# Kernel optimization log

Measured on AMD Instinct MI355X. Metric: run time of the kernel, lower is better.

The kernel has to match this reference:

```python
import jax, jax.numpy as jnp
import numpy as np

B, S, D, H, NUM_LABELS = 16, 1024, 1024, 16, 3
LN_EPS = 1e-5


def setup_inputs() -> dict:
    key = jax.random.key(0)
    ks = iter(jax.random.split(key, 16))

    def w(shape, k):
        return jax.random.normal(k, shape, jnp.float32) * 0.02

    inp = {}
    inp["embedded"] = jax.random.normal(next(ks), (B, S, D), jnp.float32)
    inp["attention_mask"] = jnp.ones((B, S), jnp.float32)
    for pfx in ("p2h", "h2p"):
        for name in ("q", "k", "v", "o"):
            inp[f"{pfx}_W{name}"] = w((D, D), next(ks))
            inp[f"{pfx}_b{name}"] = jnp.zeros((D,), jnp.float32)
        inp[f"{pfx}_ln_g"] = jnp.ones((D,), jnp.float32)
        inp[f"{pfx}_ln_b"] = jnp.zeros((D,), jnp.float32)
    inp["W1"] = w((4 * D, D), next(ks)); inp["b1"] = jnp.zeros((D,), jnp.float32)
    inp["W2"] = w((D, D // 2), next(ks)); inp["b2"] = jnp.zeros((D // 2,), jnp.float32)
    inp["W3"] = w((D // 2, NUM_LABELS), next(ks)); inp["b3"] = jnp.zeros((NUM_LABELS,), jnp.float32)
    return inp


def _layernorm(x, g, b):
    mu = jnp.mean(x, axis=-1, keepdims=True)
    var = jnp.mean(jnp.square(x - mu), axis=-1, keepdims=True)
    return (x - mu) / jnp.sqrt(var + LN_EPS) * g + b


def _cross_attn(q_in, kv_in, kv_mask, Wq, bq, Wk, bk, Wv, bv, Wo, bo, g, bln):
    Bs, Sq, Dm = q_in.shape
    Sk = kv_in.shape[1]
    hd = Dm // H
    Q = (q_in @ Wq + bq).reshape(Bs, Sq, H, hd)
    K = (kv_in @ Wk + bk).reshape(Bs, Sk, H, hd)
    V = (kv_in @ Wv + bv).reshape(Bs, Sk, H, hd)
    scores = jnp.einsum("bqhd,bkhd->bhqk", Q, K) / jnp.sqrt(jnp.float32(hd))
    scores = jnp.where(kv_mask[:, None, None, :] == 0, jnp.float32(-1e9), scores)
    wts = jax.nn.softmax(scores, axis=-1)  # dropout is identity in eval
    att = jnp.einsum("bhqk,bkhd->bqhd", wts, V).reshape(Bs, Sq, Dm)
    return _layernorm(att @ Wo + bo + q_in, g, bln)


def _pool(x, m):
    s = jnp.sum(x * m[:, :, None], axis=1)
    d = jnp.clip(jnp.sum(m, axis=1, keepdims=True), 1e-9, None)
    return s / d


def reference(embedded, attention_mask,
              p2h_Wq, p2h_bq, p2h_Wk, p2h_bk, p2h_Wv, p2h_bv, p2h_Wo, p2h_bo, p2h_ln_g, p2h_ln_b,
              h2p_Wq, h2p_bq, h2p_Wk, h2p_bk, h2p_Wv, h2p_bv, h2p_Wo, h2p_bo, h2p_ln_g, h2p_ln_b,
              W1, b1, W2, b2, W3, b3):
    half = embedded.shape[1] // 2
    premise, hypothesis = embedded[:, :half], embedded[:, half:]
    pm, hm = attention_mask[:, :half], attention_mask[:, half:]
    p2h = _cross_attn(premise, hypothesis, hm,
                      p2h_Wq, p2h_bq, p2h_Wk, p2h_bk, p2h_Wv, p2h_bv, p2h_Wo, p2h_bo, p2h_ln_g, p2h_ln_b)
    h2p = _cross_attn(hypothesis, premise, pm,
                      h2p_Wq, h2p_bq, h2p_Wk, h2p_bk, h2p_Wv, h2p_bv, h2p_Wo, h2p_bo, h2p_ln_g, h2p_ln_b)
    feats = jnp.concatenate([_pool(premise, pm), _pool(hypothesis, hm),
                             _pool(p2h, pm), _pool(h2p, hm)], axis=-1)
    h1 = jax.nn.relu(feats @ W1 + b1)
    h2 = jax.nn.relu(h1 @ W2 + b2)
    return h2 @ W3 + b3
```

## Files before the change

### kernel.cpp

```cpp
#include <hip/hip_runtime.h>
#include <hip/hip_bf16.h>

typedef __attribute__((ext_vector_type(8))) __bf16 bf16x8;
typedef __attribute__((ext_vector_type(4))) float f32x4;
typedef __attribute__((ext_vector_type(4))) int i32x4;
typedef __attribute__((ext_vector_type(4))) unsigned short u16x4;

#define MFMA16(a, b, c) __builtin_amdgcn_mfma_f32_16x16x32_bf16((a), (b), (c), 0, 0, 0)

__device__ __forceinline__ void gload_lds16(const void* g, void* l)
{
    __builtin_amdgcn_global_load_lds(
        (const __attribute__((address_space(1))) unsigned int*)g,
        (__attribute__((address_space(3))) unsigned int*)l, 16, 0, 0);
}

struct LnW { const float* g[2]; const float* b[2]; };

__global__ __launch_bounds__(256) void cast_emb_kernel(const float* __restrict__ emb,
                                                       __bf16* __restrict__ A)
{
    int i = (blockIdx.x * 256 + threadIdx.x) * 4;
    int r = i >> 10, d = i & 1023;
    size_t src = ((size_t)(r >> 9) * 1024 + (r & 511)) * 1024 + d;
    f32x4 p = *(const f32x4*)(emb + src);
    f32x4 h = *(const f32x4*)(emb + src + 512 * 1024);
    union { __bf16 b[4]; u16x4 u; } cp, ch;
#pragma unroll
    for (int j = 0; j < 4; ++j) { cp.b[j] = (__bf16)p[j]; ch.b[j] = (__bf16)h[j]; }
    *(u16x4*)(A + i) = cp.u;
    *(u16x4*)(A + 8388608 + i) = ch.u;
}

struct WPtrs { const float* p[8]; };
__global__ __launch_bounds__(256) void cast_wt_kernel(WPtrs wp, __bf16* __restrict__ Wt0)
{
    const float* W = wp.p[blockIdx.z];
    __bf16* Wt = Wt0 + (size_t)blockIdx.z * 1048576;
    __shared__ float tile[32][33];
    int n0 = blockIdx.x * 32, k0 = blockIdx.y * 32;
    int tx = threadIdx.x, ty = threadIdx.y;
#pragma unroll
    for (int i = ty; i < 32; i += 8)
        tile[i][tx] = W[(size_t)(k0 + i) * 1024 + n0 + tx];
    __syncthreads();
#pragma unroll
    for (int i = ty; i < 32; i += 8)
        Wt[(size_t)(n0 + i) * 1024 + k0 + tx] = (__bf16)tile[tx][i];
}

struct GArgs {
    const __bf16* w[2];
    const float* bias[6];
    __bf16* Qb; __bf16* Kb; __bf16* Vt;
    float* Cf; const float* resid;
};
template <int EPI>
__global__ __launch_bounds__(256, 3) void gemm_bt(const __bf16* __restrict__ A, GArgs a,
                                                  int NN)
{
    __shared__ __align__(16) __bf16 As[128 * 32];
    __shared__ __align__(16) __bf16 Bs[128 * 32];
    const int t = threadIdx.x;
    const int l = t & 63, w = t >> 6;
    const int wr = w >> 1, wc = w & 1;
    const int lrow = l & 15, lk = l >> 4;

    const int id = blockIdx.x;
    const int x = id & 7, rr = id >> 3;
    const int mblk = x * 16 + (rr & 15);
    const int nblk = rr >> 4;
    const int m0 = mblk * 128, n0 = nblk * 128;
    const int dir = mblk >> 6;
    const int seg = (EPI == 5) ? (n0 >> 10) : 0;
    const int r0 = t >> 2, kc0 = (t & 3) * 8;
    const int K = 1024;

    const int am0 = (EPI == 5 && seg != 0) ? (m0 ^ 8192) : m0;
    const __bf16* Bt = a.w[dir];
    const __bf16* gA0 = A + (size_t)(am0 + r0) * K + kc0;
    const __bf16* gA1 = gA0 + (size_t)64 * K;
    const __bf16* gB0 = Bt + (size_t)(n0 + r0) * K + kc0;
    const __bf16* gB1 = gB0 + (size_t)64 * K;
    __bf16* dA0 = &As[r0 * 32 + kc0];
    __bf16* dA1 = &As[(r0 + 64) * 32 + kc0];
    __bf16* dB0 = &Bs[r0 * 32 + kc0];
    __bf16* dB1 = &Bs[(r0 + 64) * 32 + kc0];

    const f32x4 zero = {0.f, 0.f, 0.f, 0.f};
    f32x4 acc[4][4];
#pragma unroll
    for (int mi = 0; mi < 4; ++mi)
#pragma unroll
        for (int ni = 0; ni < 4; ++ni) acc[mi][ni] = zero;

    for (int kt = 0; kt < 32; ++kt) {
        const int ko = kt * 32;
        gload_lds16(gA0 + ko, dA0);
        gload_lds16(gA1 + ko, dA1);
        gload_lds16(gB0 + ko, dB0);
        gload_lds16(gB1 + ko, dB1);
        __syncthreads();
        bf16x8 af[4], bfv[4];
#pragma unroll
        for (int mi = 0; mi < 4; ++mi)
            af[mi] = *(const bf16x8*)(&As[(wr * 64 + mi * 16 + lrow) * 32 + lk * 8]);
#pragma unroll
        for (int ni = 0; ni < 4; ++ni)
            bfv[ni] = *(const bf16x8*)(&Bs[(wc * 64 + ni * 16 + lrow) * 32 + lk * 8]);
#pragma unroll
        for (int mi = 0; mi < 4; ++mi)
#pragma unroll
            for (int ni = 0; ni < 4; ++ni)
                acc[mi][ni] = MFMA16(af[mi], bfv[ni], acc[mi][ni]);
        __syncthreads();
    }

    const float* bsel = a.bias[dir * 3 + seg];
#pragma unroll
    for (int mi = 0; mi < 4; ++mi) {
#pragma unroll
        for (int ni = 0; ni < 4; ++ni) {
            int col = n0 + wc * 64 + ni * 16 + lrow;
            int c2 = col & 1023;
            float bv = bsel[c2];
#pragma unroll
            for (int r = 0; r < 4; ++r) {
                int row = m0 + wr * 64 + mi * 16 + lk * 4 + r;
                float v = acc[mi][ni][r] + bv;
                if (EPI == 5) {
                    if (seg == 0) {
                        a.Qb[(size_t)row * 1024 + c2] = (__bf16)v;
                    } else if (seg == 1) {
                        a.Kb[(size_t)row * 1024 + c2] = (__bf16)v;
                    } else {
                        int local = row & 8191;
                        int b_ = local >> 9, pos = local & 511;
                        int h_ = c2 >> 6, hd = c2 & 63;
                        a.Vt[(size_t)dir * 8388608 +
                             (((size_t)(b_ * 16 + h_) * 64 + hd) << 9) + pos] = (__bf16)v;
                    }
                } else {
                    int local = row & 8191;
                    int b_ = local >> 9, s = local & 511;
                    float rv = a.resid[((size_t)b_ * 1024 + dir * 512 + s) * 1024 + c2];
                    a.Cf[(size_t)row * 1024 + c2] = v + rv;
                }
            }
        }
    }
}

__global__ __launch_bounds__(256, 3) void attn_kernel(const __bf16* __restrict__ Q,
                                                      const __bf16* __restrict__ Kb,
                                                      const __bf16* __restrict__ Vt,
                                                      const float* __restrict__ mask,
                                                      __bf16* __restrict__ att)
{
    __shared__ __align__(16) __bf16 KB[2][128 * 64];
    __shared__ __align__(16) __bf16 Pt[64 * 128];
    __shared__ __align__(16) float msk[512];
    const int id = blockIdx.x;
    const int xcd = id & 7, slot = id >> 3;
    const int dirbh = xcd * 64 + (slot >> 3);
    const int q0 = (slot & 7) * 64;
    const int dir = dirbh >> 8, bh = dirbh & 255;
    const int b = bh >> 4, h = bh & 15;
    const int mask_half = dir ? 0 : 512;
    const int tid = threadIdx.x, l = tid & 63, w = tid >> 6;
    const int lrow = l & 15, lk = l >> 4;
    const size_t rowbase = (size_t)dir * 8192 + b * 512;

    const __bf16* kbase = Kb + rowbase * 1024 + h * 64;
    const __bf16* vsrc = Vt + (size_t)dir * 8388608 + (size_t)bh * 64 * 512;

    auto stage = [&](int t, int buf) {
        char* dst = (char*)KB[buf];
#pragma unroll
        for (int i = 0; i < 4; ++i) {
            int c = tid + i * 256;
            int pos = c >> 3, gslot = (c & 7) ^ (pos & 7);
            gload_lds16(kbase + (size_t)(t * 128 + pos) * 1024 + gslot * 8, dst + c * 16);
        }
    };

    stage(0, 0);
    for (int i = tid; i < 512; i += 256) msk[i] = mask[b * 1024 + mask_half + i];

    const __bf16* qptr = Q + (rowbase + q0 + w * 16 + lrow) * 1024 + h * 64;
    bf16x8 qf0 = *(const bf16x8*)(qptr + lk * 8);
    bf16x8 qf1 = *(const bf16x8*)(qptr + 32 + lk * 8);

    const f32x4 zero = {0.f, 0.f, 0.f, 0.f};
    f32x4 av[4];
#pragma unroll
    for (int ni = 0; ni < 4; ++ni) av[ni] = zero;
    float m_run = -3e38f, su = 0.f;
    const int psw = lrow & 7;
    char* prowp = (char*)Pt + (w * 16 + lrow) * 256;
    f32x4 sc[8];
    bf16x8 vfr[16];

#pragma unroll
    for (int t = 0; t < 4; ++t) {
        __syncthreads();
        const char* kbuf = (const char*)KB[t & 1];
#pragma unroll
        for (int jj = 0; jj < 8; ++jj) {
            const char* kb = kbuf + (jj * 16 + lrow) * 128;
            bf16x8 k0 = *(const bf16x8*)(kb + ((lk ^ psw) << 4));
            bf16x8 k1 = *(const bf16x8*)(kb + (((lk + 4) ^ psw) << 4));
            f32x4 c = zero;
            c = MFMA16(k0, qf0, c);
            c = MFMA16(k1, qf1, c);
            sc[jj] = c;
        }
        if (t < 3) stage(t + 1, (t + 1) & 1);

        const int koff = t * 128;
#pragma unroll
        for (int ks = 0; ks < 4; ++ks)
#pragma unroll
            for (int ni = 0; ni < 4; ++ni)
                vfr[ks * 4 + ni] =
                    *(const bf16x8*)(&vsrc[(ni * 16 + lrow) * 512 + koff + ks * 32 + lk * 8]);

        float mt = -3e38f;
#pragma unroll
        for (int jj = 0; jj < 8; ++jj) {
            f32x4 mv = *(const f32x4*)(&msk[koff + jj * 16 + lk * 4]);
#pragma unroll
            for (int r = 0; r < 4; ++r) {
                float s = sc[jj][r] * 0.125f;
                if (mv[r] == 0.f) s = -1e9f;
                sc[jj][r] = s;
                mt = fmaxf(mt, s);
            }
        }
        mt = fmaxf(mt, __shfl_xor(mt, 16));
        mt = fmaxf(mt, __shfl_xor(mt, 32));
        float m_new = fmaxf(m_run, mt);
        float f = __expf(m_run - m_new);
        float s0 = 0.f, s1 = 0.f;
#pragma unroll
        for (int jj = 0; jj < 8; ++jj) {
            float e0 = __expf(sc[jj][0] - m_new);
            float e1 = __expf(sc[jj][1] - m_new);
            float e2 = __expf(sc[jj][2] - m_new);
            float e3 = __expf(sc[jj][3] - m_new);
            sc[jj][0] = e0; sc[jj][1] = e1; sc[jj][2] = e2; sc[jj][3] = e3;
            s0 += e0 + e1;
            s1 += e2 + e3;
        }
        float ssum = s0 + s1;
        ssum += __shfl_xor(ssum, 16);
        ssum += __shfl_xor(ssum, 32);
        su = su * f + ssum;
        m_run = m_new;
#pragma unroll
        for (int r = 0; r < 4; ++r) {
            float fr = __shfl(f, (l & 48) | (lk * 4 + r));
#pragma unroll
            for (int ni = 0; ni < 4; ++ni) av[ni][r] *= fr;
        }

#pragma unroll
        for (int jj = 0; jj < 8; ++jj) {
            union { __bf16 b[4]; unsigned long long u; } pk;
#pragma unroll
            for (int r = 0; r < 4; ++r) pk.b[r] = (__bf16)sc[jj][r];
            int slot2 = jj * 2 + (lk >> 1);
            *(unsigned long long*)(prowp + (((slot2 ^ psw) << 4) | ((lk & 1) << 3))) = pk.u;
        }
#pragma unroll
        for (int ks = 0; ks < 4; ++ks) {
            bf16x8 pf = *(const bf16x8*)(prowp + (((ks * 4 + lk) ^ psw) << 4));
#pragma unroll
            for (int ni = 0; ni < 4; ++ni)
                av[ni] = MFMA16(pf, vfr[ks * 4 + ni], av[ni]);
        }
    }

    const float inv = 1.f / su;
#pragma unroll
    for (int r = 0; r < 4; ++r) {
        float ivr = __shfl(inv, (l & 48) | (lk * 4 + r));
        size_t orow = rowbase + q0 + w * 16 + lk * 4 + r;
#pragma unroll
        for (int ni = 0; ni < 4; ++ni)
            att[orow * 1024 + h * 64 + ni * 16 + lrow] = (__bf16)(av[ni][r] * ivr);
    }
}

__global__ __launch_bounds__(256) void ln_stats_kernel(const float* __restrict__ X,
                                                       float2* __restrict__ stats)
{
    const int r = blockIdx.x, t = threadIdx.x;
    const float* x = X + (size_t)r * 1024;
    f32x4 v = *(const f32x4*)(x + t * 4);
    float s = v[0] + v[1] + v[2] + v[3];
    float q = v[0] * v[0] + v[1] * v[1] + v[2] * v[2] + v[3] * v[3];
#pragma unroll
    for (int d = 1; d < 64; d <<= 1) { s += __shfl_xor(s, d); q += __shfl_xor(q, d); }
    __shared__ float rs[4], rq[4];
    if ((t & 63) == 0) { rs[t >> 6] = s; rq[t >> 6] = q; }
    __syncthreads();
    if (t == 0) {
        s = rs[0] + rs[1] + rs[2] + rs[3];
        q = rq[0] + rq[1] + rq[2] + rq[3];
        float mu = s * (1.f / 1024.f);
        float var = q * (1.f / 1024.f) - mu * mu;
        stats[r] = make_float2(mu, rsqrtf(var + 1e-5f));
    }
}

__global__ __launch_bounds__(256) void pool_f32_kernel(const float* __restrict__ X,
                                                       const float* __restrict__ mask,
                                                       float* __restrict__ feats)
{
    const int b = blockIdx.y, d0 = blockIdx.x * 64, half = blockIdx.z * 512;
    const int t = threadIdx.x, d = d0 + (t & 63), sl = t >> 6;
    float acc = 0.f, ms = 0.f;
#pragma unroll 4
    for (int s = sl * 128; s < sl * 128 + 128; ++s) {
        float m = mask[b * 1024 + half + s];
        acc += X[((size_t)b * 1024 + half + s) * 1024 + d] * m;
        ms += m;
    }
    __shared__ float ra[4][64];
    __shared__ float rm[4];
    ra[sl][t & 63] = acc;
    if ((t & 63) == 0) rm[sl] = ms;
    __syncthreads();
    if (t < 64) {
        float a = ra[0][t] + ra[1][t] + ra[2][t] + ra[3][t];
        float m = rm[0] + rm[1] + rm[2] + rm[3];
        feats[b * 4096 + blockIdx.z * 1024 + d0 + t] = a / fmaxf(m, 1e-9f);
    }
}

__global__ __launch_bounds__(256) void pool_ln_kernel(const float* __restrict__ Of,
                                                      const float2* __restrict__ stats,
                                                      const float* __restrict__ mask,
                                                      LnW lw,
                                                      float* __restrict__ feats)
{
    const int b = blockIdx.y, d0 = blockIdx.x * 64, dir = blockIdx.z;
    const int half = dir * 512;
    const int t = threadIdx.x, d = d0 + (t & 63), sl = t >> 6;
    float acc = 0.f, ms = 0.f;
#pragma unroll 4
    for (int s = sl * 128; s < sl * 128 + 128; ++s) {
        float m = mask[b * 1024 + half + s];
        int row = dir * 8192 + b * 512 + s;
        float2 st = stats[row];
        float x = Of[(size_t)row * 1024 + d];
        acc += m * (x - st.x) * st.y;
        ms += m;
    }
    __shared__ float ra[4][64];
    __shared__ float rm[4];
    ra[sl][t & 63] = acc;
    if ((t & 63) == 0) rm[sl] = ms;
    __syncthreads();
    if (t < 64) {
        float a = ra[0][t] + ra[1][t] + ra[2][t] + ra[3][t];
        float m = rm[0] + rm[1] + rm[2] + rm[3];
        float g = lw.g[dir][d0 + t], bb = lw.b[dir][d0 + t];
        feats[b * 4096 + 2048 + dir * 1024 + d0 + t] = (g * a + bb * m) / fmaxf(m, 1e-9f);
    }
}

__global__ __launch_bounds__(256) void fc_init_kernel(const float* __restrict__ b1,
                                                      const float* __restrict__ b2,
                                                      float* __restrict__ h1,
                                                      float* __restrict__ h2)
{
    int i = blockIdx.x * 256 + threadIdx.x;
    if (i < 16 * 1024) h1[i] = b1[i & 1023];
    else h2[i - 16 * 1024] = b2[(i - 16 * 1024) & 511];
}

template <int CH, int RELU_IN>
__global__ __launch_bounds__(256) void fc_atomic_kernel(const float* __restrict__ in,
                                                        const float* __restrict__ W,
                                                        float* __restrict__ out,
                                                        int IF, int OF)
{
    __shared__ float ins[16 * CH];
    const int t = threadIdx.x;
    const int col = blockIdx.x * 256 + t;
    const int i0 = blockIdx.y * CH;
#pragma unroll
    for (int idx = t; idx < 16 * CH; idx += 256) {
        int b = idx / CH, i = idx % CH;
        float v = in[b * IF + i0 + i];
        if (RELU_IN) v = fmaxf(v, 0.f);
        ins[idx] = v;
    }
    __syncthreads();
    float acc[16];
#pragma unroll
    for (int b = 0; b < 16; ++b) acc[b] = 0.f;
#pragma unroll 4
    for (int i = 0; i < CH; ++i) {
        float wv = W[(size_t)(i0 + i) * OF + col];
#pragma unroll
        for (int b = 0; b < 16; ++b) acc[b] += ins[b * CH + i] * wv;
    }
#pragma unroll
    for (int b = 0; b < 16; ++b) atomicAdd(out + b * OF + col, acc[b]);
}

__global__ __launch_bounds__(64) void mlp3_kernel(const float* __restrict__ h2,
                                                  const float* __restrict__ W3,
                                                  const float* __restrict__ b3,
                                                  float* __restrict__ out)
{
    int b = blockIdx.x, t = threadIdx.x;
    float a0 = 0.f, a1 = 0.f, a2 = 0.f;
    for (int i = t; i < 512; i += 64) {
        float hv = fmaxf(h2[b * 512 + i], 0.f);
        a0 += hv * W3[i * 3 + 0];
        a1 += hv * W3[i * 3 + 1];
        a2 += hv * W3[i * 3 + 2];
    }
#pragma unroll
    for (int d = 1; d < 64; d <<= 1) {
        a0 += __shfl_xor(a0, d);
        a1 += __shfl_xor(a1, d);
        a2 += __shfl_xor(a2, d);
    }
    if (t == 0) {
        out[b * 3 + 0] = a0 + b3[0];
        out[b * 3 + 1] = a1 + b3[1];
        out[b * 3 + 2] = a2 + b3[2];
    }
}

extern "C" void kernel_launch(void* const* d_in, const int* in_sizes, int n_in,
                              void* d_out, int out_size, void* d_ws, size_t ws_size,
                              hipStream_t stream)
{
    const float* emb  = (const float*)d_in[0];
    const float* mask = (const float*)d_in[1];
    const float* W1 = (const float*)d_in[22];
    const float* b1 = (const float*)d_in[23];
    const float* W2 = (const float*)d_in[24];
    const float* b2 = (const float*)d_in[25];
    const float* W3 = (const float*)d_in[26];
    const float* b3 = (const float*)d_in[27];

    char* ws = (char*)d_ws;
    constexpr size_t MB = 1ull << 20;
    __bf16* A     = (__bf16*)(ws);
    __bf16* Wt    = (__bf16*)(ws + 32 * MB);
    __bf16* Qb    = (__bf16*)(ws + 48 * MB);
    __bf16* Kb    = (__bf16*)(ws + 80 * MB);
    __bf16* Vt    = (__bf16*)(ws + 112 * MB);
    __bf16* attb  = (__bf16*)(ws);
    float*  Of    = (float*) (ws + 48 * MB);
    float*  feats = (float*) (ws + 144 * MB);
    float*  h1    = (float*) (ws + 144 * MB + 512 * 1024);
    float*  h2    = (float*) (ws + 145 * MB);
    float2* stats = (float2*)(ws + 146 * MB);

    cast_emb_kernel<<<8192, 256, 0, stream>>>(emb, A);
    WPtrs wp;
    const int widx[8] = {2, 4, 6, 8, 12, 14, 16, 18};
    for (int i = 0; i < 8; ++i) wp.p[i] = (const float*)d_in[widx[i]];
    cast_wt_kernel<<<dim3(32, 32, 8), dim3(32, 8), 0, stream>>>(wp, Wt);

    GArgs gqkv = {}, go = {};
    LnW lw;
    for (int dir = 0; dir < 2; ++dir) {
        const int base = dir ? 12 : 2;
        gqkv.w[dir] = Wt + (size_t)(dir * 4) * 1048576;
        gqkv.bias[dir * 3 + 0] = (const float*)d_in[base + 1];
        gqkv.bias[dir * 3 + 1] = (const float*)d_in[base + 3];
        gqkv.bias[dir * 3 + 2] = (const float*)d_in[base + 5];
        go.w[dir] = Wt + (size_t)(dir * 4 + 3) * 1048576;
        go.bias[dir * 3] = (const float*)d_in[base + 7];
        lw.g[dir] = (const float*)d_in[base + 8];
        lw.b[dir] = (const float*)d_in[base + 9];
    }
    gqkv.Qb = Qb; gqkv.Kb = Kb; gqkv.Vt = Vt;
    go.Cf = Of; go.resid = emb;

    gemm_bt<5><<<3072, 256, 0, stream>>>(A, gqkv, 24);
    attn_kernel<<<4096, 256, 0, stream>>>(Qb, Kb, Vt, mask, attb);
    gemm_bt<2><<<1024, 256, 0, stream>>>(attb, go, 8);
    ln_stats_kernel<<<16384, 256, 0, stream>>>(Of, stats);
    pool_ln_kernel<<<dim3(16, 16, 2), 256, 0, stream>>>(Of, stats, mask, lw, feats);
    pool_f32_kernel<<<dim3(16, 16, 2), 256, 0, stream>>>(emb, mask, feats);

    fc_init_kernel<<<96, 256, 0, stream>>>(b1, b2, h1, h2);
    fc_atomic_kernel<128, 0><<<dim3(4, 32), 256, 0, stream>>>(feats, W1, h1, 4096, 1024);
    fc_atomic_kernel<32, 1><<<dim3(2, 32), 256, 0, stream>>>(h1, W2, h2, 1024, 512);
    mlp3_kernel<<<16, 64, 0, stream>>>(h2, W3, b3, (float*)d_out);
}
```

Before: 502.5 us.

## Replace QKV GEMM with 256x256-tile double-buffered swizzled-LDS kernel

Adds a dedicated QKV projection kernel using 256x256 output tiles, 512 threads, a K-step of 64, and double-buffered LDS with XOR swizzling. Next-tile loads are staged in four quarters interleaved with MFMA phases, and s_setprio is raised around the MFMA blocks. The aim is more data reuse per tile, fewer bank conflicts and overlap of global loads with compute. The generic gemm_bt is simplified to serve only the output projection. The trade-off is 128KB of LDS per block, which lowers occupancy, and a small grid of 768 blocks.

```diff
diff --git a/kernel.cpp b/kernel.cpp
--- a/kernel.cpp
+++ b/kernel.cpp
@@ -55,6 +55,172 @@
     __bf16* Qb; __bf16* Kb; __bf16* Vt;
     float* Cf; const float* resid;
 };
+
+__global__ __launch_bounds__(512, 2) void gemm256_qkv(const __bf16* __restrict__ A, GArgs a)
+{
+    __shared__ __align__(16) __bf16 Ab[2][256 * 64];
+    __shared__ __align__(16) __bf16 Bb[2][256 * 64];
+    const int tid = threadIdx.x, l = tid & 63;
+    const int wid = tid >> 6, wm = wid >> 2, wn = wid & 3;
+    const int lrow = l & 15, lk = l >> 4;
+
+    const int id = blockIdx.x;
+    const int x = id & 7, rr = id >> 3;
+    const int mblk = x * 8 + (rr & 7);
+    const int nblk = rr >> 3;
+    const int m0 = mblk * 256, n0 = nblk * 256;
+    const int dir = mblk >> 5;
+    const int seg = n0 >> 10;
+    const int am0 = (seg != 0) ? (m0 ^ 8192) : m0;
+    const __bf16* Ap = A + (size_t)am0 * 1024;
+    const __bf16* Bp = a.w[dir] + (size_t)n0 * 1024;
+
+    auto stage = [&](int kt, int b, int hp) {
+        const __bf16* gp = (hp < 2) ? Ap : Bp;
+        __bf16* lp = ((hp < 2) ? Ab[b] : Bb[b]) + (hp & 1) * (128 * 64);
+#pragma unroll
+        for (int i = 0; i < 2; ++i) {
+            int cc = tid + i * 512;
+            int rl = cc >> 3, sl = cc & 7;
+            int gs = sl ^ (rl & 7);
+            gload_lds16(gp + (size_t)((hp & 1) * 128 + rl) * 1024 + kt * 64 + gs * 8,
+                        lp + cc * 8);
+        }
+    };
+
+    stage(0, 0, 0); stage(0, 0, 1); stage(0, 0, 2); stage(0, 0, 3);
+
+    const f32x4 zero = {0.f, 0.f, 0.f, 0.f};
+    f32x4 acc[8][4];
+#pragma unroll
+    for (int mi = 0; mi < 8; ++mi)
+#pragma unroll
+        for (int ni = 0; ni < 4; ++ni) acc[mi][ni] = zero;
+
+    bf16x8 af[4][2], bf[2][2];
+
+    for (int kt = 0; kt < 16; ++kt) {
+        const int buf = kt & 1, nbuf = buf ^ 1;
+        const __bf16* Abuf = Ab[buf];
+        const __bf16* Bbuf = Bb[buf];
+        const int arow0 = wm * 128 + lrow;
+        const int brow0 = wn * 64 + lrow;
+
+        if (kt < 15) { stage(kt + 1, nbuf, 0);
+                       asm volatile("s_waitcnt vmcnt(2)" ::: "memory"); }
+        else         { asm volatile("s_waitcnt vmcnt(0)" ::: "memory"); }
+        __builtin_amdgcn_s_barrier();
+#pragma unroll
+        for (int mi = 0; mi < 4; ++mi) {
+            int row = arow0 + mi * 16;
+#pragma unroll
+            for (int ks = 0; ks < 2; ++ks)
+                af[mi][ks] = *(const bf16x8*)(&Abuf[row * 64 + (((ks * 4 + lk) ^ (row & 7)) * 8)]);
+        }
+#pragma unroll
+        for (int ni = 0; ni < 2; ++ni) {
+            int row = brow0 + ni * 16;
+#pragma unroll
+            for (int ks = 0; ks < 2; ++ks)
+                bf[ni][ks] = *(const bf16x8*)(&Bbuf[row * 64 + (((ks * 4 + lk) ^ (row & 7)) * 8)]);
+        }
+        __builtin_amdgcn_s_setprio(1);
+#pragma unroll
+        for (int mi = 0; mi < 4; ++mi)
+#pragma unroll
+            for (int ni = 0; ni < 2; ++ni)
+#pragma unroll
+                for (int ks = 0; ks < 2; ++ks)
+                    acc[mi][ni] = MFMA16(af[mi][ks], bf[ni][ks], acc[mi][ni]);
+        __builtin_amdgcn_s_setprio(0);
+        __builtin_amdgcn_s_barrier();
+
+        if (kt < 15) stage(kt + 1, nbuf, 1);
+#pragma unroll
+        for (int ni = 0; ni < 2; ++ni) {
+            int row = brow0 + (ni + 2) * 16;
+#pragma unroll
+            for (int ks = 0; ks < 2; ++ks)
+                bf[ni][ks] = *(const bf16x8*)(&Bbuf[row * 64 + (((ks * 4 + lk) ^ (row & 7)) * 8)]);
+        }
+        __builtin_amdgcn_s_setprio(1);
+#pragma unroll
+        for (int mi = 0; mi < 4; ++mi)
+#pragma unroll
+            for (int ni = 0; ni < 2; ++ni)
+#pragma unroll
+                for (int ks = 0; ks < 2; ++ks)
+                    acc[mi][ni + 2] = MFMA16(af[mi][ks], bf[ni][ks], acc[mi][ni + 2]);
+        __builtin_amdgcn_s_setprio(0);
+        __builtin_amdgcn_s_barrier();
+
+        if (kt < 15) stage(kt + 1, nbuf, 2);
+#pragma unroll
+        for (int mi = 0; mi < 4; ++mi) {
+            int row = arow0 + (mi + 4) * 16;
+#pragma unroll
+            for (int ks = 0; ks < 2; ++ks)
+                af[mi][ks] = *(const bf16x8*)(&Abuf[row * 64 + (((ks * 4 + lk) ^ (row & 7)) * 8)]);
+        }
+        __builtin_amdgcn_s_setprio(1);
+#pragma unroll
+        for (int mi = 0; mi < 4; ++mi)
+#pragma unroll
+            for (int ni = 0; ni < 2; ++ni)
+#pragma unroll
+                for (int ks = 0; ks < 2; ++ks)
+                    acc[mi + 4][ni + 2] = MFMA16(af[mi][ks], bf[ni][ks], acc[mi + 4][ni + 2]);
+        __builtin_amdgcn_s_setprio(0);
+        __builtin_amdgcn_s_barrier();
+
+        if (kt < 15) stage(kt + 1, nbuf, 3);
+#pragma unroll
+        for (int ni = 0; ni < 2; ++ni) {
+            int row = brow0 + ni * 16;
+#pragma unroll
+            for (int ks = 0; ks < 2; ++ks)
+                bf[ni][ks] = *(const bf16x8*)(&Bbuf[row * 64 + (((ks * 4 + lk) ^ (row & 7)) * 8)]);
+        }
+        __builtin_amdgcn_s_setprio(1);
+#pragma unroll
+        for (int mi = 0; mi < 4; ++mi)
+#pragma unroll
+            for (int ni = 0; ni < 2; ++ni)
+#pragma unroll
+                for (int ks = 0; ks < 2; ++ks)
+                    acc[mi + 4][ni] = MFMA16(af[mi][ks], bf[ni][ks], acc[mi + 4][ni]);
+        __builtin_amdgcn_s_setprio(0);
+        __builtin_amdgcn_s_barrier();
+    }
+
+    const float* bsel = a.bias[dir * 3 + seg];
+#pragma unroll
+    for (int mi = 0; mi < 8; ++mi) {
+#pragma unroll
+        for (int ni = 0; ni < 4; ++ni) {
+            int col = n0 + wn * 64 + ni * 16 + lrow;
+            int c2 = col & 1023;
+            float bv = bsel[c2];
+#pragma unroll
+            for (int r = 0; r < 4; ++r) {
+                int row = m0 + wm * 128 + mi * 16 + lk * 4 + r;
+                float v = acc[mi][ni][r] + bv;
+                if (seg == 0) {
+                    a.Qb[(size_t)row * 1024 + c2] = (__bf16)v;
+                } else if (seg == 1) {
+                    a.Kb[(size_t)row * 1024 + c2] = (__bf16)v;
+                } else {
+                    int local = row & 8191;
+                    int b_ = local >> 9, pos = local & 511;
+                    int h_ = c2 >> 6, hd = c2 & 63;
+                    a.Vt[(size_t)dir * 8388608 +
+                         (((size_t)(b_ * 16 + h_) * 64 + hd) << 9) + pos] = (__bf16)v;
+                }
+            }
+        }
+    }
+}
+
 template <int EPI>
 __global__ __launch_bounds__(256, 3) void gemm_bt(const __bf16* __restrict__ A, GArgs a,
                                                   int NN)
@@ -72,13 +238,11 @@
     const int nblk = rr >> 4;
     const int m0 = mblk * 128, n0 = nblk * 128;
     const int dir = mblk >> 6;
-    const int seg = (EPI == 5) ? (n0 >> 10) : 0;
     const int r0 = t >> 2, kc0 = (t & 3) * 8;
     const int K = 1024;
 
-    const int am0 = (EPI == 5 && seg != 0) ? (m0 ^ 8192) : m0;
     const __bf16* Bt = a.w[dir];
-    const __bf16* gA0 = A + (size_t)(am0 + r0) * K + kc0;
+    const __bf16* gA0 = A + (size_t)(m0 + r0) * K + kc0;
     const __bf16* gA1 = gA0 + (size_t)64 * K;
     const __bf16* gB0 = Bt + (size_t)(n0 + r0) * K + kc0;
     const __bf16* gB1 = gB0 + (size_t)64 * K;
@@ -116,36 +280,21 @@
         __syncthreads();
     }
 
-    const float* bsel = a.bias[dir * 3 + seg];
 #pragma unroll
     for (int mi = 0; mi < 4; ++mi) {
 #pragma unroll
         for (int ni = 0; ni < 4; ++ni) {
             int col = n0 + wc * 64 + ni * 16 + lrow;
             int c2 = col & 1023;
-            float bv = bsel[c2];
+            float bv = a.bias[dir * 3][c2];
 #pragma unroll
             for (int r = 0; r < 4; ++r) {
                 int row = m0 + wr * 64 + mi * 16 + lk * 4 + r;
                 float v = acc[mi][ni][r] + bv;
-                if (EPI == 5) {
-                    if (seg == 0) {
-                        a.Qb[(size_t)row * 1024 + c2] = (__bf16)v;
-                    } else if (seg == 1) {
-                        a.Kb[(size_t)row * 1024 + c2] = (__bf16)v;
-                    } else {
-                        int local = row & 8191;
-                        int b_ = local >> 9, pos = local & 511;
-                        int h_ = c2 >> 6, hd = c2 & 63;
-                        a.Vt[(size_t)dir * 8388608 +
-                             (((size_t)(b_ * 16 + h_) * 64 + hd) << 9) + pos] = (__bf16)v;
-                    }
-                } else {
-                    int local = row & 8191;
-                    int b_ = local >> 9, s = local & 511;
-                    float rv = a.resid[((size_t)b_ * 1024 + dir * 512 + s) * 1024 + c2];
-                    a.Cf[(size_t)row * 1024 + c2] = v + rv;
-                }
+                int local = row & 8191;
+                int b_ = local >> 9, s = local & 511;
+                float rv = a.resid[((size_t)b_ * 1024 + dir * 512 + s) * 1024 + c2];
+                a.Cf[(size_t)row * 1024 + c2] = v + rv;
             }
         }
     }
@@ -487,7 +636,7 @@
     gqkv.Qb = Qb; gqkv.Kb = Kb; gqkv.Vt = Vt;
     go.Cf = Of; go.resid = emb;
 
-    gemm_bt<5><<<3072, 256, 0, stream>>>(A, gqkv, 24);
+    gemm256_qkv<<<768, 512, 0, stream>>>(A, gqkv);
     attn_kernel<<<4096, 256, 0, stream>>>(Qb, Kb, Vt, mask, attb);
     gemm_bt<2><<<1024, 256, 0, stream>>>(attb, go, 8);
     ln_stats_kernel<<<16384, 256, 0, stream>>>(Of, stats);
```

New measurement: 532.5 us. +6.0%, slower.
